# Kernel optimization log

Measured on AMD Instinct MI355X. Metric: run time of the kernel, lower is better.

The kernel has to match this reference:

```python
import jax, jax.numpy as jnp
import numpy as np

E = 1024      # embedding_size
H = 16        # num_head
DQ = DK = DV = 64  # per-head q/k/v size


def setup_inputs() -> dict:
    key = jax.random.key(0)
    ks = jax.random.split(key, 9)
    B, S = 2, 2048
    s = 1.0 / np.sqrt(E)
    return {
        "q": jax.random.normal(ks[0], (B, S, E), jnp.float32),
        "k": jax.random.normal(ks[1], (B, S, E), jnp.float32),
        "v": jax.random.normal(ks[2], (B, S, E), jnp.float32),
        "w_q": jax.random.normal(ks[3], (E, H * DQ), jnp.float32) * s,
        "b_q": jax.random.normal(ks[4], (H * DQ,), jnp.float32) * s,
        "w_k": jax.random.normal(ks[5], (E, H * DK), jnp.float32) * s,
        "b_k": jax.random.normal(ks[6], (H * DK,), jnp.float32) * s,
        "w_v": jax.random.normal(ks[7], (E, H * DV), jnp.float32) * s,
        "b_v": jax.random.normal(ks[8], (H * DV,), jnp.float32) * s,
    }


def reference(q, k, v, w_q, b_q, w_k, b_k, w_v, b_v):
    B, Sq, _ = q.shape
    Sk = k.shape[1]
    # projections -> [B, S, H, d] -> [B, H, S, d]
    qh = (q @ w_q + b_q).reshape(B, Sq, H, DQ).transpose(0, 2, 1, 3)
    kh = (k @ w_k + b_k).reshape(B, Sk, H, DK).transpose(0, 2, 1, 3)
    vh = (v @ w_v + b_v).reshape(B, Sk, H, DV).transpose(0, 2, 1, 3)
    # scaled dot-product attention; scores [B, H, Sq, Sk]
    scores = jnp.einsum("bhqd,bhkd->bhqk", qh, kh) / jnp.sqrt(jnp.float32(DQ))
    weights = jax.nn.softmax(scores, axis=-1)
    out = jnp.einsum("bhqk,bhkd->bhqd", weights, vh)  # [B, H, Sq, DV]
    return out.transpose(0, 2, 1, 3).reshape(B, Sq, H * DV)
```

## Files before the change

### kernel.cpp

```cpp
#include <hip/hip_runtime.h>
#include <hip/hip_bf16.h>

typedef __bf16 bf16_t;
typedef bf16_t bf16x8 __attribute__((ext_vector_type(8)));
typedef bf16_t bf16x4 __attribute__((ext_vector_type(4)));
typedef short  short4v __attribute__((ext_vector_type(4)));
typedef float  f32x4  __attribute__((ext_vector_type(4)));

#define MFMA16(a,b,c) __builtin_amdgcn_mfma_f32_16x16x32_bf16(a, b, c, 0, 0, 0)

constexpr int S = 2048, H = 16, Dh = 64;
constexpr int N = H * Dh;
constexpr int K = 1024;
constexpr float QSCALE = 0.125f * 1.4426950408889634f;

static __device__ inline void load_lds16(const bf16_t* g, bf16_t* l) {
  __builtin_amdgcn_global_load_lds(
      (const __attribute__((address_space(1))) void*)g,
      (__attribute__((address_space(3))) void*)l, 16, 0, 0);
}

static __device__ inline ushort f2bb(float x) {
  bf16_t h = (bf16_t)x;
  return __builtin_bit_cast(ushort, h);
}

__global__ __launch_bounds__(256) void prep(
    const float* __restrict__ q, const float* __restrict__ k,
    const float* __restrict__ v,
    const float* __restrict__ wq, const float* __restrict__ wk,
    const float* __restrict__ wv,
    bf16_t* __restrict__ xq, bf16_t* __restrict__ xk, bf16_t* __restrict__ xv,
    bf16_t* __restrict__ wtq, bf16_t* __restrict__ wtk, bf16_t* __restrict__ wtv) {
  __shared__ ushort tile[64][68];
  int bx = blockIdx.x, t = threadIdx.x;
  if (bx < 6144) {
    int z = bx >> 11, bb = bx & 2047;
    const float* xi = z == 0 ? q : z == 1 ? k : v;
    bf16_t*      xo = z == 0 ? xq : z == 1 ? xk : xv;
    size_t idx = ((size_t)bb * 256 + t) * 8;
    float4 a = *(const float4*)&xi[idx];
    float4 b = *(const float4*)&xi[idx + 4];
    bf16x8 w;
    w[0] = (bf16_t)a.x; w[1] = (bf16_t)a.y; w[2] = (bf16_t)a.z; w[3] = (bf16_t)a.w;
    w[4] = (bf16_t)b.x; w[5] = (bf16_t)b.y; w[6] = (bf16_t)b.z; w[7] = (bf16_t)b.w;
    *(bf16x8*)&xo[idx] = w;
  } else {
    int zz = bx - 6144;
    int z = zz >> 8, bb = zz & 255;
    const float* wi = z == 0 ? wq : z == 1 ? wk : wv;
    ushort*      wo = (ushort*)(z == 0 ? wtq : z == 1 ? wtk : wtv);
    int k0 = (bb >> 4) * 64, n0 = (bb & 15) * 64;
    for (int i = 0; i < 4; ++i) {
      int idx4 = (i * 256 + t) * 4;
      int r = idx4 >> 6, c = idx4 & 63;
      float4 vv = *(const float4*)&wi[(size_t)(k0 + r) * N + n0 + c];
      tile[r][c] = f2bb(vv.x); tile[r][c + 1] = f2bb(vv.y);
      tile[r][c + 2] = f2bb(vv.z); tile[r][c + 3] = f2bb(vv.w);
    }
    __syncthreads();
    for (int i = 0; i < 4; ++i) {
      int idx4 = (i * 256 + t) * 4;
      int r = idx4 >> 6, c = idx4 & 63;
      ushort4 vv;
      vv.x = tile[c][r]; vv.y = tile[c + 1][r];
      vv.z = tile[c + 2][r]; vv.w = tile[c + 3][r];
      *(ushort4*)&wo[(size_t)(n0 + r) * K + k0 + c] = vv;
    }
  }
}

__global__ __launch_bounds__(256) void proj_gemm(
    const bf16_t* __restrict__ xq, const bf16_t* __restrict__ xk,
    const bf16_t* __restrict__ xv,
    const bf16_t* __restrict__ wtq, const bf16_t* __restrict__ wtk,
    const bf16_t* __restrict__ wtv,
    const float* __restrict__ bq, const float* __restrict__ bk,
    const float* __restrict__ bv,
    bf16_t* __restrict__ qh, bf16_t* __restrict__ kh, bf16_t* __restrict__ vt) {
  int bid = blockIdx.x;
  int logical = (bid & 7) * 96 + (bid >> 3);
  int mode = logical >> 8;
  int rem = logical & 255;
  int gx = rem & 7;
  int gy = rem >> 3;

  const bf16_t* X  = mode == 0 ? xq  : mode == 1 ? xk  : wtv;
  const bf16_t* Wt = mode == 0 ? wtq : mode == 1 ? wtk : xv;
  const float*  Bi = mode == 0 ? bq  : mode == 1 ? bk  : bv;

  __shared__ __align__(16) bf16_t smem[17408];
  bf16_t (*Ash)[64] = (bf16_t(*)[64])smem;
  bf16_t (*Bsh)[64] = (bf16_t(*)[64])(smem + 8192);
  bf16_t* Cs = smem;

  int tid = threadIdx.x;
  int wave = tid >> 6, lane = tid & 63;
  int lr = lane & 15, lg = lane >> 4;
  int lrow = lane >> 3, lchunk = lane & 7;
  int m0 = (mode < 2 ? gy : gx) * 128;
  int n0 = (mode < 2 ? gx : gy) * 128;
  int wm = (wave >> 1) * 64, wn = (wave & 1) * 64;

  f32x4 acc[4][4];
  for (int i = 0; i < 4; ++i)
    for (int j = 0; j < 4; ++j) acc[i][j] = (f32x4){0.f, 0.f, 0.f, 0.f};

  for (int ko = 0; ko < K / 64; ++ko) {
    __syncthreads();
    for (int j = 0; j < 4; ++j) {
      int r = wave * 32 + j * 8 + lrow;
      int gc = (lchunk ^ (r & 7)) * 8;
      load_lds16(&X [(size_t)(m0 + r) * K + ko * 64 + gc], &Ash[r][lchunk * 8]);
      load_lds16(&Wt[(size_t)(n0 + r) * K + ko * 64 + gc], &Bsh[r][lchunk * 8]);
    }
    __syncthreads();
    for (int kk = 0; kk < 2; ++kk) {
      bf16x8 af[4], bfr[4];
      for (int i = 0; i < 4; ++i) {
        int rr = wm + i * 16 + lr;
        af[i] = *(const bf16x8*)&Ash[rr][(((kk << 2) | lg) ^ (rr & 7)) * 8];
      }
      for (int j = 0; j < 4; ++j) {
        int rr = wn + j * 16 + lr;
        bfr[j] = *(const bf16x8*)&Bsh[rr][(((kk << 2) | lg) ^ (rr & 7)) * 8];
      }
      for (int i = 0; i < 4; ++i)
        for (int j = 0; j < 4; ++j)
          acc[i][j] = MFMA16(af[i], bfr[j], acc[i][j]);
    }
  }

  float badd[4][4][4];
  if (mode < 2) {
    float bvv[4];
    for (int j = 0; j < 4; ++j) bvv[j] = Bi[n0 + wn + j * 16 + lr];
    for (int i = 0; i < 4; ++i)
      for (int j = 0; j < 4; ++j)
        for (int r = 0; r < 4; ++r) badd[i][j][r] = bvv[j];
  } else {
    for (int i = 0; i < 4; ++i)
      for (int r = 0; r < 4; ++r) {
        float bm = Bi[m0 + wm + i * 16 + lg * 4 + r];
        for (int j = 0; j < 4; ++j) badd[i][j][r] = bm;
      }
  }

  __syncthreads();
  for (int i = 0; i < 4; ++i)
    for (int j = 0; j < 4; ++j)
      for (int r = 0; r < 4; ++r) {
        float vvv = acc[i][j][r] + badd[i][j][r];
        if (mode == 0) vvv *= QSCALE;
        Cs[(size_t)(wm + i * 16 + lg * 4 + r) * 136 + wn + j * 16 + lr] = (bf16_t)vvv;
      }
  __syncthreads();

  bf16_t* o = mode == 0 ? qh : mode == 1 ? kh : vt;
  for (int p = 0; p < 8; ++p) {
    int idx = p * 256 + tid;
    int row = idx >> 4, ch = idx & 15;
    bf16x8 vv = *(const bf16x8*)&Cs[(size_t)row * 136 + ch * 8];
    size_t dst;
    if (mode < 2) {
      int m_g = m0 + row, n_g = n0 + ch * 8;
      int b = m_g >> 11, s = m_g & 2047;
      int h = n_g >> 6, d = n_g & 63;
      dst = (((size_t)(b * 16 + h) * 2048) + s) * 64 + d;
    } else {
      int w_g = m0 + row, t_g = n0 + ch * 8;
      int b = t_g >> 11, s = t_g & 2047;
      dst = ((size_t)(b * 1024 + w_g)) * 2048 + s;
    }
    *(uint4*)&o[dst] = __builtin_bit_cast(uint4, vv);
  }
}

__global__ __launch_bounds__(512, 2) void attn(
    const bf16_t* __restrict__ qh, const bf16_t* __restrict__ kh,
    const bf16_t* __restrict__ vt, float* __restrict__ out) {
  __shared__ __align__(16) bf16_t smem[16640];

  int tid = threadIdx.x, wave = tid >> 6, lane = tid & 63;
  int lr = lane & 15, lg = lane >> 4;
  int half = wave >> 2, w4 = wave & 3;

  int bid = blockIdx.x;
  int logical = (bid & 7) * 64 + (bid >> 3);
  int bh = logical >> 4;
  int q0 = (logical & 15) * 128 + w4 * 32;

  bf16_t* vb = smem + half * 4096;

  const bf16_t* qg = qh + (size_t)bh * S * Dh;
  const bf16_t* kg = kh + (size_t)bh * S * Dh;
  const bf16_t* vg = vt + (size_t)bh * Dh * S;

  bf16x8 bqf[2][2];
#pragma unroll
  for (int ms = 0; ms < 2; ++ms)
#pragma unroll
    for (int kk = 0; kk < 2; ++kk)
      bqf[ms][kk] = *(const bf16x8*)
          &qg[(size_t)(q0 + ms * 16 + lr) * 64 + kk * 32 + lg * 8];

  bf16x8 ones8;
#pragma unroll
  for (int j = 0; j < 8; ++j) ones8[j] = (bf16_t)1.0f;

  f32x4 o_acc[2][4], lacc[2];
#pragma unroll
  for (int ms = 0; ms < 2; ++ms) {
    lacc[ms] = (f32x4){0.f, 0.f, 0.f, 0.f};
#pragma unroll
    for (int dt = 0; dt < 4; ++dt) o_acc[ms][dt] = (f32x4){0.f, 0.f, 0.f, 0.f};
  }

  int lrow = lane >> 3, lchunk = lane & 7;
  int srow0 = w4 * 16 + lrow;
  int srow1 = srow0 + 8;
  int sgc = (lchunk ^ (srow0 & 7)) * 8;
  int ld0 = srow0 * 64 + lchunk * 8;
  int ld1 = ld0 + 512;

  int cb = half * (S / 2);

  uint4 vr0 = *(const uint4*)&vg[(size_t)srow0 * S + cb + sgc];
  uint4 vr1 = *(const uint4*)&vg[(size_t)srow1 * S + cb + sgc];
  *(uint4*)&vb[ld0] = vr0;
  *(uint4*)&vb[ld1] = vr1;
  {
    int sk1 = cb + 64;
    vr0 = *(const uint4*)&vg[(size_t)srow0 * S + sk1 + sgc];
    vr1 = *(const uint4*)&vg[(size_t)srow1 * S + sk1 + sgc];
  }

  int sw = lr & 7, p4 = (lg & 1) * 4;

  constexpr int NITH = (S / 2) / 64;
  for (int it = 0; it < NITH; ++it) {
    bf16x8 ak[4][2];
#pragma unroll
    for (int t = 0; t < 4; ++t)
#pragma unroll
      for (int kk = 0; kk < 2; ++kk)
        ak[t][kk] = *(const bf16x8*)
            &kg[(size_t)(cb + it * 64 + t * 16 + lr) * 64 + kk * 32 + lg * 8];

    __syncthreads();
    if (it + 1 < NITH) {
      bf16_t* w = vb + ((it + 1) & 1) * 8192;
      *(uint4*)&w[ld0] = vr0;
      *(uint4*)&w[ld1] = vr1;
      if (it + 2 < NITH) {
        int sk = cb + (it + 2) * 64;
        vr0 = *(const uint4*)&vg[(size_t)srow0 * S + sk + sgc];
        vr1 = *(const uint4*)&vg[(size_t)srow1 * S + sk + sgc];
      }
    }
    const bf16_t* vsr = vb + (it & 1) * 8192;

    bf16x8 pa8[2][2];
#pragma unroll
    for (int tp = 0; tp < 2; ++tp) {
      f32x4 st[2][2];
#pragma unroll
      for (int ms = 0; ms < 2; ++ms)
#pragma unroll
        for (int ts = 0; ts < 2; ++ts) st[ms][ts] = (f32x4){0.f, 0.f, 0.f, 0.f};
#pragma unroll
      for (int ts = 0; ts < 2; ++ts) {
        int t = tp * 2 + ts;
#pragma unroll
        for (int ms = 0; ms < 2; ++ms) {
          st[ms][ts] = MFMA16(ak[t][0], bqf[ms][0], st[ms][ts]);
          st[ms][ts] = MFMA16(ak[t][1], bqf[ms][1], st[ms][ts]);
        }
      }
#pragma unroll
      for (int ms = 0; ms < 2; ++ms)
#pragma unroll
        for (int r = 0; r < 4; ++r) {
          pa8[ms][tp][r]     = (bf16_t)__builtin_amdgcn_exp2f(st[ms][0][r]);
          pa8[ms][tp][r + 4] = (bf16_t)__builtin_amdgcn_exp2f(st[ms][1][r]);
        }
    }

#pragma unroll
    for (int tp = 0; tp < 2; ++tp) {
      int g0 = tp * 4 + (lg >> 1);
#pragma unroll
      for (int dt = 0; dt < 4; ++dt) {
        const bf16_t* vrow = &vsr[(dt * 16 + lr) * 64];
        bf16x4 lo = *(const bf16x4*)&vrow[((g0      ^ sw) * 8) + p4];
        bf16x4 hi = *(const bf16x4*)&vrow[(((g0 + 2) ^ sw) * 8) + p4];
        bf16x8 bb;
#pragma unroll
        for (int j = 0; j < 4; ++j) { bb[j] = lo[j]; bb[j + 4] = hi[j]; }
#pragma unroll
        for (int ms = 0; ms < 2; ++ms)
          o_acc[ms][dt] = MFMA16(pa8[ms][tp], bb, o_acc[ms][dt]);
      }
#pragma unroll
      for (int ms = 0; ms < 2; ++ms)
        lacc[ms] = MFMA16(pa8[ms][tp], ones8, lacc[ms]);
    }
  }

  __syncthreads();
  float* mo = (float*)smem;
  float* ls = mo + 8 * 16 * 64;

  if (half == 1) {
#pragma unroll
    for (int ms = 0; ms < 2; ++ms)
#pragma unroll
      for (int r = 0; r < 4; ++r) {
        int row = (w4 * 2 + ms) * 16 + lg * 4 + r;
#pragma unroll
        for (int dt = 0; dt < 4; ++dt)
          mo[row * 64 + dt * 16 + lr] = o_acc[ms][dt][r];
        if (lr == 0) ls[row] = lacc[ms][r];
      }
  }
  __syncthreads();
  if (half == 0) {
    int b = bh >> 4, hh = bh & 15;
#pragma unroll
    for (int ms = 0; ms < 2; ++ms)
#pragma unroll
      for (int r = 0; r < 4; ++r) {
        int row = (w4 * 2 + ms) * 16 + lg * 4 + r;
        float inv = 1.f / (lacc[ms][r] + ls[row]);
        int s_row = q0 + ms * 16 + lg * 4 + r;
        size_t base = ((size_t)(b * S + s_row)) * 1024 + hh * 64;
#pragma unroll
        for (int dt = 0; dt < 4; ++dt)
          out[base + dt * 16 + lr] =
              (o_acc[ms][dt][r] + mo[row * 64 + dt * 16 + lr]) * inv;
      }
  }
}

extern "C" void kernel_launch(void* const* d_in, const int* in_sizes, int n_in,
                              void* d_out, int out_size, void* d_ws, size_t ws_size,
                              hipStream_t stream) {
  const float* q  = (const float*)d_in[0];
  const float* k  = (const float*)d_in[1];
  const float* v  = (const float*)d_in[2];
  const float* wq = (const float*)d_in[3];
  const float* bq = (const float*)d_in[4];
  const float* wk = (const float*)d_in[5];
  const float* bk = (const float*)d_in[6];
  const float* wv = (const float*)d_in[7];
  const float* bv = (const float*)d_in[8];

  bf16_t* ws  = (bf16_t*)d_ws;
  constexpr size_t MW = (size_t)1 << 20;
  constexpr size_t MX = (size_t)4096 * 1024;
  bf16_t* wtq = ws;
  bf16_t* wtk = wtq + MW;
  bf16_t* wtv = wtk + MW;
  bf16_t* xq  = wtv + MW;
  bf16_t* xk  = xq + MX;
  bf16_t* xv  = xk + MX;
  bf16_t* qhd = xv + MX;
  bf16_t* khd = qhd + MX;
  bf16_t* vtd = khd + MX;
  float* out  = (float*)d_out;

  prep<<<6912, 256, 0, stream>>>(q, k, v, wq, wk, wv,
                                 xq, xk, xv, wtq, wtk, wtv);
  proj_gemm<<<768, 256, 0, stream>>>(xq, xk, xv, wtq, wtk, wtv,
                                     bq, bk, bv, qhd, khd, vtd);
  attn<<<512, 512, 0, stream>>>(qhd, khd, vtd, out);
}
```

Before: 218.4 us.

## Double-buffer K fragments in registers and prefetch the next tile during PV

The attention loop is unrolled by two with ping-pong register buffers for the K fragments. The next K tile is loaded from global memory after the QK/exp phase and before the PV phase, so its latency overlaps with the PV MFMAs instead of stalling the start of each iteration. This adds a second set of K registers, which raises register pressure at 2 blocks of 512 threads per CU and could force spills.

```diff
diff --git a/kernel.cpp b/kernel.cpp
--- a/kernel.cpp
+++ b/kernel.cpp
@@ -176,6 +176,67 @@
   }
 }
 
+static __device__ __forceinline__ void load_ak(
+    bf16x8 (&ak)[4][2], const bf16_t* kbase, int tile) {
+#pragma unroll
+  for (int t = 0; t < 4; ++t)
+#pragma unroll
+    for (int kk = 0; kk < 2; ++kk)
+      ak[t][kk] = *(const bf16x8*)&kbase[tile * 4096 + t * 1024 + kk * 32];
+}
+
+static __device__ __forceinline__ void qk_phase(
+    const bf16x8 (&ak)[4][2], const bf16x8 (&bqf)[2][2], bf16x8 (&pa8)[2][2]) {
+#pragma unroll
+  for (int tp = 0; tp < 2; ++tp) {
+    f32x4 st[2][2];
+#pragma unroll
+    for (int ms = 0; ms < 2; ++ms)
+#pragma unroll
+      for (int ts = 0; ts < 2; ++ts) st[ms][ts] = (f32x4){0.f, 0.f, 0.f, 0.f};
+#pragma unroll
+    for (int ts = 0; ts < 2; ++ts) {
+      int t = tp * 2 + ts;
+#pragma unroll
+      for (int ms = 0; ms < 2; ++ms) {
+        st[ms][ts] = MFMA16(ak[t][0], bqf[ms][0], st[ms][ts]);
+        st[ms][ts] = MFMA16(ak[t][1], bqf[ms][1], st[ms][ts]);
+      }
+    }
+#pragma unroll
+    for (int ms = 0; ms < 2; ++ms)
+#pragma unroll
+      for (int r = 0; r < 4; ++r) {
+        pa8[ms][tp][r]     = (bf16_t)__builtin_amdgcn_exp2f(st[ms][0][r]);
+        pa8[ms][tp][r + 4] = (bf16_t)__builtin_amdgcn_exp2f(st[ms][1][r]);
+      }
+  }
+}
+
+static __device__ __forceinline__ void pv_phase(
+    const bf16_t* vsr, const bf16x8 (&pa8)[2][2], const bf16x8& ones8,
+    f32x4 (&o_acc)[2][4], f32x4 (&lacc)[2], int lr, int lg, int sw, int p4) {
+#pragma unroll
+  for (int tp = 0; tp < 2; ++tp) {
+    int g0 = tp * 4 + (lg >> 1);
+#pragma unroll
+    for (int dt = 0; dt < 4; ++dt) {
+      const bf16_t* vrow = &vsr[(dt * 16 + lr) * 64];
+      bf16x4 lo = *(const bf16x4*)&vrow[((g0      ^ sw) * 8) + p4];
+      bf16x4 hi = *(const bf16x4*)&vrow[(((g0 + 2) ^ sw) * 8) + p4];
+      bf16x8 bb;
+#pragma unroll
+      for (int j = 0; j < 4; ++j) { bb[j] = lo[j]; bb[j + 4] = hi[j]; }
+#pragma unroll
+      for (int ms = 0; ms < 2; ++ms)
+        o_acc[ms][dt] = MFMA16(pa8[ms][tp], bb, o_acc[ms][dt]);
+    }
+#pragma unroll
+    for (int ms = 0; ms < 2; ++ms)
+      lacc[ms] = MFMA16(pa8[ms][tp], ones8, lacc[ms]);
+  }
+}
+
 __global__ __launch_bounds__(512, 2) void attn(
     const bf16_t* __restrict__ qh, const bf16_t* __restrict__ kh,
     const bf16_t* __restrict__ vt, float* __restrict__ out) {
@@ -224,6 +285,9 @@
   int ld1 = ld0 + 512;
 
   int cb = half * (S / 2);
+  int sw = lr & 7, p4 = (lg & 1) * 4;
+
+  const bf16_t* kbase = kg + ((size_t)cb + lr) * 64 + lg * 8;
 
   uint4 vr0 = *(const uint4*)&vg[(size_t)srow0 * S + cb + sgc];
   uint4 vr1 = *(const uint4*)&vg[(size_t)srow1 * S + cb + sgc];
@@ -234,76 +298,47 @@
     vr0 = *(const uint4*)&vg[(size_t)srow0 * S + sk1 + sgc];
     vr1 = *(const uint4*)&vg[(size_t)srow1 * S + sk1 + sgc];
   }
-
-  int sw = lr & 7, p4 = (lg & 1) * 4;
+  bf16x8 akA[4][2], akB[4][2];
+  load_ak(akA, kbase, 0);
 
   constexpr int NITH = (S / 2) / 64;
-  for (int it = 0; it < NITH; ++it) {
-    bf16x8 ak[4][2];
-#pragma unroll
-    for (int t = 0; t < 4; ++t)
-#pragma unroll
-      for (int kk = 0; kk < 2; ++kk)
-        ak[t][kk] = *(const bf16x8*)
-            &kg[(size_t)(cb + it * 64 + t * 16 + lr) * 64 + kk * 32 + lg * 8];
-
-    __syncthreads();
-    if (it + 1 < NITH) {
-      bf16_t* w = vb + ((it + 1) & 1) * 8192;
-      *(uint4*)&w[ld0] = vr0;
-      *(uint4*)&w[ld1] = vr1;
-      if (it + 2 < NITH) {
-        int sk = cb + (it + 2) * 64;
-        vr0 = *(const uint4*)&vg[(size_t)srow0 * S + sk + sgc];
-        vr1 = *(const uint4*)&vg[(size_t)srow1 * S + sk + sgc];
-      }
-    }
-    const bf16_t* vsr = vb + (it & 1) * 8192;
-
-    bf16x8 pa8[2][2];
-#pragma unroll
-    for (int tp = 0; tp < 2; ++tp) {
-      f32x4 st[2][2];
-#pragma unroll
-      for (int ms = 0; ms < 2; ++ms)
-#pragma unroll
-        for (int ts = 0; ts < 2; ++ts) st[ms][ts] = (f32x4){0.f, 0.f, 0.f, 0.f};
-#pragma unroll
-      for (int ts = 0; ts < 2; ++ts) {
-        int t = tp * 2 + ts;
-#pragma unroll
-        for (int ms = 0; ms < 2; ++ms) {
-          st[ms][ts] = MFMA16(ak[t][0], bqf[ms][0], st[ms][ts]);
-          st[ms][ts] = MFMA16(ak[t][1], bqf[ms][1], st[ms][ts]);
+#pragma unroll 1
+  for (int it2 = 0; it2 < NITH / 2; ++it2) {
+    {
+      int it = 2 * it2;
+      __syncthreads();
+      {
+        bf16_t* w = vb + 8192;
+        *(uint4*)&w[ld0] = vr0;
+        *(uint4*)&w[ld1] = vr1;
+        if (it + 2 < NITH) {
+          int sk = cb + (it + 2) * 64;
+          vr0 = *(const uint4*)&vg[(size_t)srow0 * S + sk + sgc];
+          vr1 = *(const uint4*)&vg[(size_t)srow1 * S + sk + sgc];
         }
       }
-#pragma unroll
-      for (int ms = 0; ms < 2; ++ms)
-#pragma unroll
-        for (int r = 0; r < 4; ++r) {
-          pa8[ms][tp][r]     = (bf16_t)__builtin_amdgcn_exp2f(st[ms][0][r]);
-          pa8[ms][tp][r + 4] = (bf16_t)__builtin_amdgcn_exp2f(st[ms][1][r]);
+      bf16x8 pa8[2][2];
+      qk_phase(akA, bqf, pa8);
+      load_ak(akB, kbase, it + 1);
+      pv_phase(vb, pa8, ones8, o_acc, lacc, lr, lg, sw, p4);
+    }
+    {
+      int it = 2 * it2 + 1;
+      __syncthreads();
+      if (it + 1 < NITH) {
+        *(uint4*)&vb[ld0] = vr0;
+        *(uint4*)&vb[ld1] = vr1;
+        if (it + 2 < NITH) {
+          int sk = cb + (it + 2) * 64;
+          vr0 = *(const uint4*)&vg[(size_t)srow0 * S + sk + sgc];
+          vr1 = *(const uint4*)&vg[(size_t)srow1 * S + sk + sgc];
         }
-    }
-
-#pragma unroll
-    for (int tp = 0; tp < 2; ++tp) {
-      int g0 = tp * 4 + (lg >> 1);
-#pragma unroll
-      for (int dt = 0; dt < 4; ++dt) {
-        const bf16_t* vrow = &vsr[(dt * 16 + lr) * 64];
-        bf16x4 lo = *(const bf16x4*)&vrow[((g0      ^ sw) * 8) + p4];
-        bf16x4 hi = *(const bf16x4*)&vrow[(((g0 + 2) ^ sw) * 8) + p4];
-        bf16x8 bb;
-#pragma unroll
-        for (int j = 0; j < 4; ++j) { bb[j] = lo[j]; bb[j + 4] = hi[j]; }
-#pragma unroll
-        for (int ms = 0; ms < 2; ++ms)
-          o_acc[ms][dt] = MFMA16(pa8[ms][tp], bb, o_acc[ms][dt]);
-      }
-#pragma unroll
-      for (int ms = 0; ms < 2; ++ms)
-        lacc[ms] = MFMA16(pa8[ms][tp], ones8, lacc[ms]);
+      }
+      bf16x8 pa8[2][2];
+      qk_phase(akB, bqf, pa8);
+      if (it + 1 < NITH)
+        load_ak(akA, kbase, it + 1);
+      pv_phase(vb + 8192, pa8, ones8, o_acc, lacc, lr, lg, sw, p4);
     }
   }
 
```

After: 229.8 us. 1.05x slower.
